# Kernel optimization log

Measured on AMD Instinct MI355X. Metric: run time of the kernel, lower is better.

## Reference

```python
import jax, jax.numpy as jnp
import numpy as np
from jax.scipy.special import logsumexp

NEG = -1.0e7  # -QUASI_INF
B, T = 8, 16
QALL, QRES, QARG = 256, 128, 192
STATE, VOCAB = 256, 10000


def setup_inputs() -> dict:
    key = jax.random.key(0)
    ks = jax.random.split(key, 24)
    def rn(k, shape, s=0.1):
        return jax.random.normal(k, shape, dtype=jnp.float32) * s
    z = lambda *s: jnp.zeros(s, jnp.float32)
    return {
        "words": jax.random.randint(ks[0], (B, T), 0, VOCAB),
        "nt_emb": rn(ks[1], (QALL, STATE), 1.0),
        "W_emit": rn(ks[2], (STATE, VOCAB)),
        "b_emit": z(VOCAB),
        "rule_W": rn(ks[3], (QRES, 2 * QARG)),
        "rule_b": z(2 * QARG),
        "assoc": rn(ks[4], (QRES, QARG)),
        "root_w": rn(ks[5], (QALL,)),
        "root_b": z(QALL),
        "sw1": rn(ks[6], (STATE, STATE)), "sb1": z(STATE),
        "r1w1": rn(ks[7], (STATE, STATE)), "r1b1": z(STATE),
        "r1w2": rn(ks[8], (STATE, STATE)), "r1b2": z(STATE),
        "r2w1": rn(ks[9], (STATE, STATE)), "r2b1": z(STATE),
        "r2w2": rn(ks[10], (STATE, STATE)), "r2b2": z(STATE),
        "sw2": rn(ks[11], (STATE, 2)), "sb2": z(2),
        "lfunc_ixs": jax.random.randint(ks[12], (QRES, QARG), 0, QALL),
        "rfunc_ixs": jax.random.randint(ks[13], (QRES, QARG), 0, QALL),
        "argpc_2_pc": jax.random.randint(ks[14], (QARG,), 0, QALL),
        "res_2_all": jnp.arange(QRES, dtype=jnp.int32),
        "larg_mask": z(QRES, QARG),
        "rarg_mask": z(QRES, QARG),
    }


def _residual(x, w1, b1, w2, b2):
    return x + jax.nn.relu(jax.nn.relu(x @ w1 + b1) @ w2 + b2)


def _forward(words, nt_emb, W_emit, b_emit, rule_W, rule_b, assoc, root_w, root_b,
             sw1, sb1, r1w1, r1b1, r1w2, r1b2, r2w1, r2b1, r2w2, r2b2, sw2, sb2,
             lfunc_ixs, rfunc_ixs, argpc_2_pc, res_2_all, larg_mask, rarg_mask):
    Bb, Tt = words.shape
    qall = nt_emb.shape[0]
    qres, qarg = assoc.shape
    # rule_mlp applied to fake_emb = eye(qres): logits are just W + b, then log-softmax
    G = jax.nn.log_softmax(rule_W + rule_b, axis=-1) + jnp.concatenate([assoc, assoc], axis=1)
    G_larg = G[:, :qarg] + larg_mask   # argument child on the left
    G_rarg = G[:, qarg:] + rarg_mask   # argument child on the right
    # split/emit binary decision per category (split_mlp over nt_emb)
    h = nt_emb @ sw1 + sb1
    h = _residual(h, r1w1, r1b1, r1w2, r1b2)
    h = _residual(h, r2w1, r2b1, r2w2, r2b2)
    split_scores = jax.nn.log_softmax(h @ sw2 + sb2, axis=-1)  # [qall, 2]
    # emission log-probs (word model: dense projection + log-softmax over vocab)
    emit_lp = jax.nn.log_softmax(nt_emb @ W_emit + b_emit, axis=-1)  # [qall, V]
    term = jnp.moveaxis(emit_lp[:, words], 0, -1) + split_scores[:, 1]  # [B, T, qall]
    # inside chart: chart[len-1, start] -> [B, qall] log inside scores
    chart = jnp.full((Tt, Tt, Bb, qall), NEG, dtype=jnp.float32)
    chart = chart.at[0].set(jnp.swapaxes(term, 0, 1))
    split0 = split_scores[res_2_all, 0]  # split prob of result predcats
    for ell in range(2, Tt + 1):  # DP recurrence over span length (structural)
        n = Tt - ell + 1
        kk = np.arange(1, ell)
        st = np.arange(n)
        lefts = chart[kk - 1, :n]  # [S, n, B, qall]
        rights = chart[(ell - kk - 1)[:, None], st[None, :] + kk[:, None]]  # [S, n, B, qall]
        # functor on left, argument on right: lfunc_ixs[res,arg] -> functor predcat
        sc1 = lefts[..., lfunc_ixs] + rights[..., argpc_2_pc][..., None, :] + G_rarg
        # argument on left, functor on right
        sc2 = lefts[..., argpc_2_pc][..., None, :] + rights[..., rfunc_ixs] + G_larg
        parent = jnp.logaddexp(logsumexp(sc1, axis=(0, 4)), logsumexp(sc2, axis=(0, 4)))  # [n, B, qres]
        parent = parent + split0
        full = jnp.full((n, Bb, qall), NEG, dtype=jnp.float32).at[:, :, res_2_all].set(parent)
        chart = chart.at[ell - 1, :n].set(full)
    root_lp = jax.nn.log_softmax(root_w + root_b)  # root_mlp over eye(1)
    return logsumexp(chart[Tt - 1, 0] + root_lp, axis=-1)  # [B] sentence log-likelihoods


def reference(words, nt_emb, W_emit, b_emit, rule_W, rule_b, assoc, root_w, root_b,
              sw1, sb1, r1w1, r1b1, r1w2, r1b2, r2w1, r2b1, r2w2, r2b2, sw2, sb2,
              lfunc_ixs, rfunc_ixs, argpc_2_pc, res_2_all, larg_mask, rarg_mask):
    return _forward(words, nt_emb, W_emit, b_emit, rule_W, rule_b, assoc, root_w, root_b,
                    sw1, sb1, r1w1, r1b1, r1w2, r1b2, r2w1, r2b1, r2w2, r2b2, sw2, sb2,
                    lfunc_ixs, rfunc_ixs, argpc_2_pc, res_2_all, larg_mask, rarg_mask)
```

## Files before the change

kernel.cpp:

```cpp
#include <hip/hip_runtime.h>
#include <math.h>

#define NEGV -10000000.0f

constexpr int B_ = 8, T_ = 16;
constexpr int QALL = 256, QRES = 128, QARG = 192;
constexpr int STATE = 256, VOCAB = 10000;
constexpr int WT = 64;
constexpr int NWT = (VOCAB + WT - 1) / WT;
constexpr int JS = 4;

constexpr size_t OFF_CHART = 0;
constexpr size_t CHART_SZ  = (size_t)T_ * T_ * B_ * QALL;
constexpr size_t OFF_EGR   = OFF_CHART + CHART_SZ;
constexpr size_t OFF_EGL   = OFF_EGR + (size_t)QARG * QRES;
constexpr size_t OFF_LF    = OFF_EGL + (size_t)QARG * QRES;
constexpr size_t OFF_RF    = OFF_LF + (size_t)QARG * QRES;
constexpr size_t OFF_S0    = OFF_RF + (size_t)QARG * QRES;
constexpr size_t OFF_S1    = OFF_S0 + QALL;
constexpr size_t OFF_LSE   = OFF_S1 + QALL;
constexpr size_t OFF_PMIT  = OFF_LSE + QALL;
constexpr size_t OFF_PSEM  = OFF_PMIT + (size_t)NWT * QALL;
constexpr int    PMAXP     = 704;
constexpr size_t OFF_P0S   = OFF_PMIT;
constexpr size_t OFF_P0M   = OFF_P0S + (size_t)PMAXP * QRES;
constexpr size_t OFF_P1S   = OFF_P0M + PMAXP;
constexpr size_t OFF_P1M   = OFF_P1S + (size_t)PMAXP * QRES;
constexpr size_t OFF_RAW   = OFF_P1S;

__device__ __forceinline__ size_t chIdx(int ell, int s, int b) {
    return OFF_CHART + ((size_t)((ell * 16 + s) * 8 + b)) * 256;
}

__device__ __forceinline__ float waveMax(float v) {
    #pragma unroll
    for (int m = 32; m >= 1; m >>= 1) v = fmaxf(v, __shfl_xor(v, m, 64));
    return v;
}
__device__ __forceinline__ float waveSum(float v) {
    #pragma unroll
    for (int m = 32; m >= 1; m >>= 1) v += __shfl_xor(v, m, 64);
    return v;
}
__device__ __forceinline__ float blockMax(float v, float* scr, int nw) {
    int lane = threadIdx.x & 63, w = threadIdx.x >> 6;
    v = waveMax(v);
    if (lane == 0) scr[w] = v;
    __syncthreads();
    float r = scr[0];
    for (int i = 1; i < nw; i++) r = fmaxf(r, scr[i]);
    __syncthreads();
    return r;
}
__device__ __forceinline__ float blockSum(float v, float* scr, int nw) {
    int lane = threadIdx.x & 63, w = threadIdx.x >> 6;
    v = waveSum(v);
    if (lane == 0) scr[w] = v;
    __syncthreads();
    float r = 0.f;
    for (int i = 0; i < nw; i++) r += scr[i];
    __syncthreads();
    return r;
}

__global__ __launch_bounds__(192) void prep_g_kernel(
        const float* __restrict__ rule_W, const float* __restrict__ rule_b,
        const float* __restrict__ assoc,
        const float* __restrict__ larg_mask, const float* __restrict__ rarg_mask,
        const int* __restrict__ lfunc, const int* __restrict__ rfunc,
        float* __restrict__ ws) {
    __shared__ float scr[4];
    int r = blockIdx.x;
    int j = threadIdx.x;
    float v0 = rule_W[r * 2 * QARG + j] + rule_b[j];
    float v1 = rule_W[r * 2 * QARG + QARG + j] + rule_b[QARG + j];
    float m = blockMax(fmaxf(v0, v1), scr, 3);
    float s = blockSum(expf(v0 - m) + expf(v1 - m), scr, 3);
    float l = m + logf(s);
    float av = assoc[r * QARG + j];
    float gl = v0 - l + av + larg_mask[r * QARG + j];
    float gr = v1 - l + av + rarg_mask[r * QARG + j];
    ws[OFF_EGL + (size_t)j * QRES + r] = expf(gl);
    ws[OFF_EGR + (size_t)j * QRES + r] = expf(gr);
    ((int*)ws)[OFF_LF + (size_t)j * QRES + r] = lfunc[r * QARG + j];
    ((int*)ws)[OFF_RF + (size_t)j * QRES + r] = rfunc[r * QARG + j];
}

#define MLP_MATVEC(INBUF, W, RES) do {                                          \
    float acc_ = 0.f;                                                           \
    _Pragma("unroll 16")                                                        \
    for (int s_ = 0; s_ < 64; s_++)                                             \
        acc_ += INBUF[s0 + s_] * W[(s0 + s_) * STATE + col];                    \
    part[t] = acc_;                                                             \
    __syncthreads();                                                            \
    RES = part[col] + part[STATE + col] + part[2 * STATE + col]                 \
        + part[3 * STATE + col];                                                \
} while (0)

__global__ __launch_bounds__(1024) void mlp_kernel(
        const float* __restrict__ nt_emb,
        const float* __restrict__ sw1, const float* __restrict__ sb1,
        const float* __restrict__ r1w1, const float* __restrict__ r1b1,
        const float* __restrict__ r1w2, const float* __restrict__ r1b2,
        const float* __restrict__ r2w1, const float* __restrict__ r2b1,
        const float* __restrict__ r2w2, const float* __restrict__ r2b2,
        const float* __restrict__ sw2, const float* __restrict__ sb2,
        float* __restrict__ ws) {
    __shared__ float xin[STATE], hbuf[STATE], tbuf[STATE];
    __shared__ float part[4 * STATE];
    __shared__ float scr[16];
    int a = blockIdx.x, t = threadIdx.x;
    int col = t & 255;
    int grp = t >> 8;
    int s0 = grp * 64;
    if (t < STATE) xin[t] = nt_emb[a * STATE + t];
    __syncthreads();
    float r;
    MLP_MATVEC(xin, sw1, r);
    if (grp == 0) hbuf[col] = r + sb1[col];
    __syncthreads();
    MLP_MATVEC(hbuf, r1w1, r);
    if (grp == 0) tbuf[col] = fmaxf(r + r1b1[col], 0.f);
    __syncthreads();
    MLP_MATVEC(tbuf, r1w2, r);
    if (grp == 0) hbuf[col] += fmaxf(r + r1b2[col], 0.f);
    __syncthreads();
    MLP_MATVEC(hbuf, r2w1, r);
    if (grp == 0) tbuf[col] = fmaxf(r + r2b1[col], 0.f);
    __syncthreads();
    MLP_MATVEC(tbuf, r2w2, r);
    if (grp == 0) hbuf[col] += fmaxf(r + r2b2[col], 0.f);
    __syncthreads();
    float hv = (t < STATE) ? hbuf[t] : 0.f;
    float v0 = (t < STATE) ? hv * sw2[t * 2 + 0] : 0.f;
    float v1 = (t < STATE) ? hv * sw2[t * 2 + 1] : 0.f;
    float u0 = blockSum(v0, scr, 16) + sb2[0];
    float u1 = blockSum(v1, scr, 16) + sb2[1];
    if (t == 0) {
        float mm = fmaxf(u0, u1);
        float l = mm + logf(expf(u0 - mm) + expf(u1 - mm));
        ws[OFF_S0 + a] = u0 - l;
        ws[OFF_S1 + a] = u1 - l;
    }
}

__global__ __launch_bounds__(256) void emit_kernel(
        const int* __restrict__ words,
        const float* __restrict__ nt_emb, const float* __restrict__ W_emit,
        const float* __restrict__ b_emit, float* __restrict__ ws) {
    __shared__ float As[2][16][64];
    __shared__ float Bs[2][16][64];
    __shared__ float redM[64][16], redS[64][16];
    __shared__ int sw[128];
    int wt = blockIdx.x, at = blockIdx.y;
    int t = threadIdx.x;
    int tx = t & 15, ty = t >> 4;
    if (t < 128) sw[t] = words[t];
    int wbase = wt * WT, abase = at * 64;
    int idx = t * 4;
    int akk = idx & 15, aaa = idx >> 4;
    int bkk = idx >> 6, bww = idx & 63;
    const float* Aptr = &nt_emb[(size_t)(abase + aaa) * STATE + akk];
    int bw = wbase + bww;
    bool bfull = (bw + 3 < VOCAB);

    {
        float4 av = *(const float4*)(Aptr + 0);
        float4 bv;
        const float* src = &W_emit[(size_t)bkk * VOCAB + bw];
        if (bfull) bv = *(const float4*)src;
        else {
            float tv[4];
            #pragma unroll
            for (int q = 0; q < 4; q++) tv[q] = (bw + q < VOCAB) ? src[q] : 0.f;
            bv = make_float4(tv[0], tv[1], tv[2], tv[3]);
        }
        As[0][akk + 0][aaa] = av.x; As[0][akk + 1][aaa] = av.y;
        As[0][akk + 2][aaa] = av.z; As[0][akk + 3][aaa] = av.w;
        *(float4*)&Bs[0][bkk][bww] = bv;
    }
    __syncthreads();

    float acc[4][4];
    #pragma unroll
    for (int i = 0; i < 4; i++)
        #pragma unroll
        for (int j = 0; j < 4; j++) acc[i][j] = 0.f;

    for (int step = 0; step < 16; step++) {
        int cur = step & 1;
        float4 nav, nbv;
        bool more = (step + 1 < 16);
        if (more) {
            nav = *(const float4*)(Aptr + (step + 1) * 16);
            const float* src = &W_emit[(size_t)((step + 1) * 16 + bkk) * VOCAB + bw];
            if (bfull) nbv = *(const float4*)src;
            else {
                float tv[4];
                #pragma unroll
                for (int q = 0; q < 4; q++) tv[q] = (bw + q < VOCAB) ? src[q] : 0.f;
                nbv = make_float4(tv[0], tv[1], tv[2], tv[3]);
            }
        }
        #pragma unroll
        for (int kk = 0; kk < 16; kk++) {
            float a4[4], b4[4];
            #pragma unroll
            for (int i = 0; i < 4; i++) a4[i] = As[cur][kk][ty * 4 + i];
            #pragma unroll
            for (int j = 0; j < 4; j++) b4[j] = Bs[cur][kk][tx * 4 + j];
            #pragma unroll
            for (int i = 0; i < 4; i++)
                #pragma unroll
                for (int j = 0; j < 4; j++) acc[i][j] += a4[i] * b4[j];
        }
        if (more) {
            int nb = cur ^ 1;
            As[nb][akk + 0][aaa] = nav.x; As[nb][akk + 1][aaa] = nav.y;
            As[nb][akk + 2][aaa] = nav.z; As[nb][akk + 3][aaa] = nav.w;
            *(float4*)&Bs[nb][bkk][bww] = nbv;
        }
        __syncthreads();
    }

    float be[4];
    #pragma unroll
    for (int j = 0; j < 4; j++) {
        int w = wbase + tx * 4 + j;
        be[j] = (w < VOCAB) ? b_emit[w] : 0.f;
    }
    #pragma unroll
    for (int i = 0; i < 4; i++)
        #pragma unroll
        for (int j = 0; j < 4; j++) {
            int w = wbase + tx * 4 + j;
            if (w < VOCAB) acc[i][j] += be[j];
        }
    for (int i2 = 0; i2 < 128; i2++) {
        int loc = sw[i2] - wbase;
        if (loc >= 0 && loc < WT && (loc >> 2) == tx) {
            int j = loc & 3;
            #pragma unroll
            for (int i = 0; i < 4; i++)
                ws[OFF_RAW + (size_t)i2 * QALL + abase + ty * 4 + i] = acc[i][j];
        }
    }
    #pragma unroll
    for (int i = 0; i < 4; i++) {
        float mloc = -3.0e38f;
        #pragma unroll
        for (int j = 0; j < 4; j++) {
            int w = wbase + tx * 4 + j;
            if (w < VOCAB) mloc = fmaxf(mloc, acc[i][j]);
        }
        float sloc = 0.f;
        #pragma unroll
        for (int j = 0; j < 4; j++) {
            int w = wbase + tx * 4 + j;
            if (w < VOCAB) sloc += expf(acc[i][j] - mloc);
        }
        redM[ty * 4 + i][tx] = mloc;
        redS[ty * 4 + i][tx] = sloc;
    }
    __syncthreads();
    if (t < 64) {
        float M = -3.0e38f;
        #pragma unroll
        for (int i = 0; i < 16; i++) M = fmaxf(M, redM[t][i]);
        float S = 0.f;
        #pragma unroll
        for (int i = 0; i < 16; i++) S += redS[t][i] * expf(redM[t][i] - M);
        ws[OFF_PMIT + (size_t)wt * QALL + abase + t] = M;
        ws[OFF_PSEM + (size_t)wt * QALL + abase + t] = S;
    }
}

__global__ __launch_bounds__(256) void lse_kernel(float* __restrict__ ws) {
    int a = threadIdx.x;
    float M = -3.0e38f;
    for (int wt = 0; wt < NWT; wt++) M = fmaxf(M, ws[OFF_PMIT + (size_t)wt * QALL + a]);
    float S = 0.f;
    for (int wt = 0; wt < NWT; wt++)
        S += ws[OFF_PSEM + (size_t)wt * QALL + a] * expf(ws[OFF_PMIT + (size_t)wt * QALL + a] - M);
    ws[OFF_LSE + a] = M + logf(S);
}

__global__ __launch_bounds__(256) void chart0_kernel(float* __restrict__ ws) {
    int blk = blockIdx.x;
    int b = blk >> 4, tp = blk & 15;
    int a = threadIdx.x;
    float val = ws[OFF_RAW + (size_t)blk * QALL + a] - ws[OFF_LSE + a] + ws[OFF_S1 + a];
    ws[chIdx(0, tp, b) + a] = val;
}

__device__ __forceinline__ void reconRow(float* row, const float* __restrict__ ws,
                                         size_t prevS, size_t prevM, int cellp, int KCp,
                                         const int* __restrict__ res2all) {
    int t = threadIdx.x;
    int np = JS * KCp;
    size_t base = (size_t)cellp * np;
    if (t < 256) row[t] = NEGV;
    float M = -3.0e38f;
    for (int p = 0; p < np; p++) M = fmaxf(M, ws[prevM + base + p]);
    __syncthreads();
    if (t < QRES) {
        float S = 0.f;
        for (int p = 0; p < np; p++)
            S += expf(ws[prevM + base + p] - M) * ws[prevS + (base + p) * QRES + t];
        row[res2all[t]] = logf(S) + M + ws[OFF_S0 + res2all[t]];
    }
    __syncthreads();
}

template<int ELL>
__global__ __launch_bounds__(512) void level_k(float* __restrict__ ws,
                                               const int* __restrict__ argpc,
                                               const int* __restrict__ res2all) {
    __shared__ __align__(16) float rowL[4][256], rowR[4][256];
    __shared__ __align__(16) float eB0[4][48], eB1[4][48];
    __shared__ float mLs[4], mRs[4];
    __shared__ float Sred[512];
    __shared__ float outrow[256];

    constexpr int K = ELL - 1;
    constexpr int KC = (K + 3) >> 2;
    constexpr int matCount = (ELL >= 3) ? (T_ - ELL + 2) * 8 : 0;
    constexpr int ellp = ELL - 1;
    constexpr int KCp = (ellp - 1 + 3) >> 2;
    constexpr size_t prevS = (ellp & 1) ? OFF_P1S : OFF_P0S;
    constexpr size_t prevM = (ellp & 1) ? OFF_P1M : OFF_P0M;
    constexpr size_t curS  = (ELL & 1) ? OFF_P1S : OFF_P0S;
    constexpr size_t curM  = (ELL & 1) ? OFF_P1M : OFF_P0M;

    int t = threadIdx.x;
    int bid = blockIdx.x;

    if (bid < matCount) {
        int cellp = bid;
        int sp = cellp >> 3, bp = cellp & 7;
        reconRow(outrow, ws, prevS, prevM, cellp, KCp, res2all);
        if (t < 256) ws[chIdx(ellp - 1, sp, bp) + t] = outrow[t];
        return;
    }

    int aid = bid - matCount;
    int kc = aid % KC;
    int rem = aid / KC;
    int jq = rem & (JS - 1);
    int cell = rem >> 2;
    int s = cell >> 3, b = cell & 7;
    int k0 = kc * 4 + 1;
    int kn = min(4, K - kc * 4);
    int j0 = jq * 48;
    int side = t >> 8, u = t & 255;

    for (int kp = 0; kp < kn; kp++) {
        int k = k0 + kp;
        bool Lprev = (ELL >= 3) && (k == K);
        bool Rprev = (ELL >= 3) && (k == 1);
        if (!Lprev && side == 0) rowL[kp][u] = ws[chIdx(k - 1, s, b) + u];
        if (!Rprev && side == 1) rowR[kp][u] = ws[chIdx(ELL - k - 1, s + k, b) + u];
    }
    for (int kp = 0; kp < kn; kp++) {
        int k = k0 + kp;
        if ((ELL >= 3) && (k == K)) reconRow(&rowL[kp][0], ws, prevS, prevM, s * 8 + b, KCp, res2all);
        if ((ELL >= 3) && (k == 1)) reconRow(&rowR[kp][0], ws, prevS, prevM, (s + 1) * 8 + b, KCp, res2all);
    }
    __syncthreads();

    int w = t >> 6, lane = t & 63;
    if (w < 2 * kn) {
        int kp = w >> 1;
        const float* pr = (w & 1) ? &rowR[kp][0] : &rowL[kp][0];
        float v = fmaxf(fmaxf(pr[lane], pr[lane + 64]), fmaxf(pr[lane + 128], pr[lane + 192]));
        v = waveMax(v);
        if (lane == 0) { if (w & 1) mRs[kp] = v; else mLs[kp] = v; }
    }
    __syncthreads();
    float mc = -3.0e38f;
    for (int kp = 0; kp < kn; kp++) mc = fmaxf(mc, mLs[kp] + mRs[kp]);

    {
        int kp = t >> 7;
        int jj = t & 127;
        if (kp < kn) {
            if (jj < 48) {
                int ap = argpc[j0 + jj];
                eB0[kp][jj] = expf(rowR[kp][ap] - (mc - mLs[kp]));
            } else if (jj >= 64 && jj < 112) {
                int j2 = jj - 64;
                int ap = argpc[j0 + j2];
                eB1[kp][j2] = expf(rowL[kp][ap] - (mc - mRs[kp]));
            }
        }
    }
    __syncthreads();

    for (int kp = 0; kp < kn; kp++) {
        if (side == 0) rowL[kp][u] = expf(rowL[kp][u] - mLs[kp]);
        else           rowR[kp][u] = expf(rowR[kp][u] - mRs[kp]);
    }
    __syncthreads();

    int r = t & 127, sub = t >> 7;
    int which = sub >> 1;
    int jbase = (sub & 1) * 24;
    const float* eGT = ws + (which == 0 ? OFF_EGR : OFF_EGL);
    const int* idxT = ((const int*)ws) + (which == 0 ? OFF_LF : OFF_RF);
    const float (*gA)[256] = which ? rowR : rowL;
    const float (*gB)[48]  = which ? eB1 : eB0;
    float acc = 0.f;
    for (int jc = 0; jc < 24; jc += 4) {
        int jj = jbase + jc;
        int j = j0 + jj;
        float g0 = eGT[(size_t)(j + 0) * QRES + r];
        float g1 = eGT[(size_t)(j + 1) * QRES + r];
        float g2 = eGT[(size_t)(j + 2) * QRES + r];
        float g3 = eGT[(size_t)(j + 3) * QRES + r];
        int i0 = idxT[(size_t)(j + 0) * QRES + r];
        int i1 = idxT[(size_t)(j + 1) * QRES + r];
        int i2 = idxT[(size_t)(j + 2) * QRES + r];
        int i3 = idxT[(size_t)(j + 3) * QRES + r];
        float t0 = 0.f, t1 = 0.f, t2 = 0.f, t3 = 0.f;
        for (int kp = 0; kp < kn; kp++) {
            const float* gs = gA[kp];
            float4 e4 = *(const float4*)&gB[kp][jj];
            t0 += gs[i0] * e4.x;
            t1 += gs[i1] * e4.y;
            t2 += gs[i2] * e4.z;
            t3 += gs[i3] * e4.w;
        }
        acc += g0 * t0 + g1 * t1 + g2 * t2 + g3 * t3;
    }
    Sred[t] = acc;
    __syncthreads();
    if (t < QRES) {
        float S = Sred[t] + Sred[128 + t] + Sred[256 + t] + Sred[384 + t];
        ws[curS + (size_t)aid * QRES + t] = S;
    }
    if (t == 0) ws[curM + aid] = mc;
}

__global__ __launch_bounds__(256) void root_kernel(const float* __restrict__ root_w,
                                                   const float* __restrict__ root_b,
                                                   const float* __restrict__ ws,
                                                   const int* __restrict__ res2all,
                                                   float* __restrict__ out) {
    int b = blockIdx.x, t = threadIdx.x;
    __shared__ float scr[4];
    __shared__ float outrow[256];
    {
        int np = JS * 4;
        size_t base = (size_t)b * np;
        outrow[t] = NEGV;
        float M = -3.0e38f;
        for (int p = 0; p < np; p++) M = fmaxf(M, ws[OFF_P0M + base + p]);
        __syncthreads();
        if (t < QRES) {
            float S = 0.f;
            for (int p = 0; p < np; p++)
                S += expf(ws[OFF_P0M + base + p] - M) * ws[OFF_P0S + (base + p) * QRES + t];
            outrow[res2all[t]] = logf(S) + M + ws[OFF_S0 + res2all[t]];
        }
        __syncthreads();
    }
    float rv = root_w[t] + root_b[t];
    float mroot = blockMax(rv, scr, 4);
    float sroot = blockSum(expf(rv - mroot), scr, 4);
    float lroot = mroot + logf(sroot);
    float v = outrow[t] + rv - lroot;
    float m2 = blockMax(v, scr, 4);
    float s2 = blockSum(expf(v - m2), scr, 4);
    if (t == 0) out[b] = m2 + logf(s2);
}

template<int ELL>
static inline void launch_level(float* ws, const int* argpc, const int* res2all,
                                hipStream_t stream) {
    constexpr int n = T_ - ELL + 1;
    constexpr int K = ELL - 1, KC = (K + 3) / 4;
    constexpr int matCount = (ELL >= 3) ? (n + 1) * 8 : 0;
    constexpr int accCount = n * 8 * JS * KC;
    level_k<ELL><<<dim3(matCount + accCount), dim3(512), 0, stream>>>(ws, argpc, res2all);
}

extern "C" void kernel_launch(void* const* d_in, const int* in_sizes, int n_in,
                              void* d_out, int out_size, void* d_ws, size_t ws_size,
                              hipStream_t stream) {
    const int*   words   = (const int*)  d_in[0];
    const float* nt_emb  = (const float*)d_in[1];
    const float* W_emit  = (const float*)d_in[2];
    const float* b_emit  = (const float*)d_in[3];
    const float* rule_W  = (const float*)d_in[4];
    const float* rule_b  = (const float*)d_in[5];
    const float* assoc   = (const float*)d_in[6];
    const float* root_w  = (const float*)d_in[7];
    const float* root_b  = (const float*)d_in[8];
    const float* sw1     = (const float*)d_in[9];
    const float* sb1     = (const float*)d_in[10];
    const float* r1w1    = (const float*)d_in[11];
    const float* r1b1    = (const float*)d_in[12];
    const float* r1w2    = (const float*)d_in[13];
    const float* r1b2    = (const float*)d_in[14];
    const float* r2w1    = (const float*)d_in[15];
    const float* r2b1    = (const float*)d_in[16];
    const float* r2w2    = (const float*)d_in[17];
    const float* r2b2    = (const float*)d_in[18];
    const float* sw2     = (const float*)d_in[19];
    const float* sb2     = (const float*)d_in[20];
    const int*   lfunc   = (const int*)  d_in[21];
    const int*   rfunc   = (const int*)  d_in[22];
    const int*   argpc   = (const int*)  d_in[23];
    const int*   res2all = (const int*)  d_in[24];
    const float* larg_m  = (const float*)d_in[25];
    const float* rarg_m  = (const float*)d_in[26];
    float* ws  = (float*)d_ws;
    float* out = (float*)d_out;

    prep_g_kernel<<<dim3(QRES), dim3(QARG), 0, stream>>>(rule_W, rule_b, assoc, larg_m, rarg_m,
                                                         lfunc, rfunc, ws);
    mlp_kernel<<<dim3(QALL), dim3(1024), 0, stream>>>(nt_emb, sw1, sb1, r1w1, r1b1, r1w2, r1b2,
                                                      r2w1, r2b1, r2w2, r2b2, sw2, sb2, ws);
    emit_kernel<<<dim3(NWT, QALL / 64), dim3(256), 0, stream>>>(words, nt_emb, W_emit, b_emit, ws);
    lse_kernel<<<dim3(1), dim3(256), 0, stream>>>(ws);
    chart0_kernel<<<dim3(B_ * T_), dim3(256), 0, stream>>>(ws);

    launch_level<2>(ws, argpc, res2all, stream);
    launch_level<3>(ws, argpc, res2all, stream);
    launch_level<4>(ws, argpc, res2all, stream);
    launch_level<5>(ws, argpc, res2all, stream);
    launch_level<6>(ws, argpc, res2all, stream);
    launch_level<7>(ws, argpc, res2all, stream);
    launch_level<8>(ws, argpc, res2all, stream);
    launch_level<9>(ws, argpc, res2all, stream);
    launch_level<10>(ws, argpc, res2all, stream);
    launch_level<11>(ws, argpc, res2all, stream);
    launch_level<12>(ws, argpc, res2all, stream);
    launch_level<13>(ws, argpc, res2all, stream);
    launch_level<14>(ws, argpc, res2all, stream);
    launch_level<15>(ws, argpc, res2all, stream);
    launch_level<16>(ws, argpc, res2all, stream);

    root_kernel<<<dim3(B_), dim3(256), 0, stream>>>(root_w, root_b, ws, res2all, out);
}
```

Before: 367.5 us.

## Fuse prep/MLP and lse/chart0 kernels, hoist G loads into registers

Merges the rule-prep kernel into the MLP kernel as extra blocks and folds the single-block LSE reduction into chart0, so two kernel launches and their serialization points disappear. Each chart0 block now recomputes the LSE over all vocab tiles, which duplicates that reduction 128 times. In the level kernel, the G/index gathers and argpc loads are hoisted into registers before the row loads, overlapping global latency with earlier work. reconRow is also templated on the partial count so its loops can be unrolled. The register arrays raise register pressure.

```diff
diff --git a/kernel.cpp b/kernel.cpp
--- a/kernel.cpp
+++ b/kernel.cpp
@@ -63,29 +63,6 @@
     return r;
 }
 
-__global__ __launch_bounds__(192) void prep_g_kernel(
-        const float* __restrict__ rule_W, const float* __restrict__ rule_b,
-        const float* __restrict__ assoc,
-        const float* __restrict__ larg_mask, const float* __restrict__ rarg_mask,
-        const int* __restrict__ lfunc, const int* __restrict__ rfunc,
-        float* __restrict__ ws) {
-    __shared__ float scr[4];
-    int r = blockIdx.x;
-    int j = threadIdx.x;
-    float v0 = rule_W[r * 2 * QARG + j] + rule_b[j];
-    float v1 = rule_W[r * 2 * QARG + QARG + j] + rule_b[QARG + j];
-    float m = blockMax(fmaxf(v0, v1), scr, 3);
-    float s = blockSum(expf(v0 - m) + expf(v1 - m), scr, 3);
-    float l = m + logf(s);
-    float av = assoc[r * QARG + j];
-    float gl = v0 - l + av + larg_mask[r * QARG + j];
-    float gr = v1 - l + av + rarg_mask[r * QARG + j];
-    ws[OFF_EGL + (size_t)j * QRES + r] = expf(gl);
-    ws[OFF_EGR + (size_t)j * QRES + r] = expf(gr);
-    ((int*)ws)[OFF_LF + (size_t)j * QRES + r] = lfunc[r * QARG + j];
-    ((int*)ws)[OFF_RF + (size_t)j * QRES + r] = rfunc[r * QARG + j];
-}
-
 #define MLP_MATVEC(INBUF, W, RES) do {                                          \
     float acc_ = 0.f;                                                           \
     _Pragma("unroll 16")                                                        \
@@ -97,7 +74,7 @@
         + part[3 * STATE + col];                                                \
 } while (0)
 
-__global__ __launch_bounds__(1024) void mlp_kernel(
+__global__ __launch_bounds__(1024) void pre_kernel(
         const float* __restrict__ nt_emb,
         const float* __restrict__ sw1, const float* __restrict__ sb1,
         const float* __restrict__ r1w1, const float* __restrict__ r1b1,
@@ -105,42 +82,69 @@
         const float* __restrict__ r2w1, const float* __restrict__ r2b1,
         const float* __restrict__ r2w2, const float* __restrict__ r2b2,
         const float* __restrict__ sw2, const float* __restrict__ sb2,
+        const float* __restrict__ rule_W, const float* __restrict__ rule_b,
+        const float* __restrict__ assoc,
+        const float* __restrict__ larg_mask, const float* __restrict__ rarg_mask,
+        const int* __restrict__ lfunc, const int* __restrict__ rfunc,
         float* __restrict__ ws) {
     __shared__ float xin[STATE], hbuf[STATE], tbuf[STATE];
     __shared__ float part[4 * STATE];
     __shared__ float scr[16];
-    int a = blockIdx.x, t = threadIdx.x;
-    int col = t & 255;
-    int grp = t >> 8;
-    int s0 = grp * 64;
-    if (t < STATE) xin[t] = nt_emb[a * STATE + t];
-    __syncthreads();
-    float r;
-    MLP_MATVEC(xin, sw1, r);
-    if (grp == 0) hbuf[col] = r + sb1[col];
-    __syncthreads();
-    MLP_MATVEC(hbuf, r1w1, r);
-    if (grp == 0) tbuf[col] = fmaxf(r + r1b1[col], 0.f);
-    __syncthreads();
-    MLP_MATVEC(tbuf, r1w2, r);
-    if (grp == 0) hbuf[col] += fmaxf(r + r1b2[col], 0.f);
-    __syncthreads();
-    MLP_MATVEC(hbuf, r2w1, r);
-    if (grp == 0) tbuf[col] = fmaxf(r + r2b1[col], 0.f);
-    __syncthreads();
-    MLP_MATVEC(tbuf, r2w2, r);
-    if (grp == 0) hbuf[col] += fmaxf(r + r2b2[col], 0.f);
-    __syncthreads();
-    float hv = (t < STATE) ? hbuf[t] : 0.f;
-    float v0 = (t < STATE) ? hv * sw2[t * 2 + 0] : 0.f;
-    float v1 = (t < STATE) ? hv * sw2[t * 2 + 1] : 0.f;
-    float u0 = blockSum(v0, scr, 16) + sb2[0];
-    float u1 = blockSum(v1, scr, 16) + sb2[1];
-    if (t == 0) {
-        float mm = fmaxf(u0, u1);
-        float l = mm + logf(expf(u0 - mm) + expf(u1 - mm));
-        ws[OFF_S0 + a] = u0 - l;
-        ws[OFF_S1 + a] = u1 - l;
+    int t = threadIdx.x;
+    if (blockIdx.x < QALL) {
+        int a = blockIdx.x;
+        int col = t & 255;
+        int grp = t >> 8;
+        int s0 = grp * 64;
+        if (t < STATE) xin[t] = nt_emb[a * STATE + t];
+        __syncthreads();
+        float r;
+        MLP_MATVEC(xin, sw1, r);
+        if (grp == 0) hbuf[col] = r + sb1[col];
+        __syncthreads();
+        MLP_MATVEC(hbuf, r1w1, r);
+        if (grp == 0) tbuf[col] = fmaxf(r + r1b1[col], 0.f);
+        __syncthreads();
+        MLP_MATVEC(tbuf, r1w2, r);
+        if (grp == 0) hbuf[col] += fmaxf(r + r1b2[col], 0.f);
+        __syncthreads();
+        MLP_MATVEC(hbuf, r2w1, r);
+        if (grp == 0) tbuf[col] = fmaxf(r + r2b1[col], 0.f);
+        __syncthreads();
+        MLP_MATVEC(tbuf, r2w2, r);
+        if (grp == 0) hbuf[col] += fmaxf(r + r2b2[col], 0.f);
+        __syncthreads();
+        float hv = (t < STATE) ? hbuf[t] : 0.f;
+        float v0 = (t < STATE) ? hv * sw2[t * 2 + 0] : 0.f;
+        float v1 = (t < STATE) ? hv * sw2[t * 2 + 1] : 0.f;
+        float u0 = blockSum(v0, scr, 16) + sb2[0];
+        float u1 = blockSum(v1, scr, 16) + sb2[1];
+        if (t == 0) {
+            float mm = fmaxf(u0, u1);
+            float l = mm + logf(expf(u0 - mm) + expf(u1 - mm));
+            ws[OFF_S0 + a] = u0 - l;
+            ws[OFF_S1 + a] = u1 - l;
+        }
+    } else {
+        int r = blockIdx.x - QALL;
+        int j = t;
+        float v0 = -3.0e38f, v1 = -3.0e38f;
+        if (t < QARG) {
+            v0 = rule_W[r * 2 * QARG + j] + rule_b[j];
+            v1 = rule_W[r * 2 * QARG + QARG + j] + rule_b[QARG + j];
+        }
+        float m = blockMax(fmaxf(v0, v1), scr, 16);
+        float s = blockSum((t < QARG) ? (expf(v0 - m) + expf(v1 - m)) : 0.f, scr, 16);
+        if (t < QARG) {
+            float l = m + logf(s);
+            float av = assoc[r * QARG + j];
+            float gl = v0 - l + av + larg_mask[r * QARG + j];
+            float gr = v1 - l + av + rarg_mask[r * QARG + j];
+            ws[OFF_EGL + (size_t)j * QRES + r] = expf(gl);
+            ws[OFF_EGR + (size_t)j * QRES + r] = expf(gr);
+            ((int*)ws)[OFF_LF + (size_t)j * QRES + r] = lfunc[r * QARG + j];
+            ((int*)ws)[OFF_RF + (size_t)j * QRES + r] = rfunc[r * QARG + j];
+        }
     }
 }
 
@@ -275,38 +279,39 @@
     }
 }
 
-__global__ __launch_bounds__(256) void lse_kernel(float* __restrict__ ws) {
+__global__ __launch_bounds__(256) void chart0_kernel(float* __restrict__ ws) {
+    int blk = blockIdx.x;
+    int b = blk >> 4, tp = blk & 15;
     int a = threadIdx.x;
     float M = -3.0e38f;
     for (int wt = 0; wt < NWT; wt++) M = fmaxf(M, ws[OFF_PMIT + (size_t)wt * QALL + a]);
     float S = 0.f;
     for (int wt = 0; wt < NWT; wt++)
         S += ws[OFF_PSEM + (size_t)wt * QALL + a] * expf(ws[OFF_PMIT + (size_t)wt * QALL + a] - M);
-    ws[OFF_LSE + a] = M + logf(S);
-}
-
-__global__ __launch_bounds__(256) void chart0_kernel(float* __restrict__ ws) {
-    int blk = blockIdx.x;
-    int b = blk >> 4, tp = blk & 15;
-    int a = threadIdx.x;
-    float val = ws[OFF_RAW + (size_t)blk * QALL + a] - ws[OFF_LSE + a] + ws[OFF_S1 + a];
+    float lse = M + logf(S);
+    float val = ws[OFF_RAW + (size_t)blk * QALL + a] - lse + ws[OFF_S1 + a];
     ws[chIdx(0, tp, b) + a] = val;
 }
 
+template<int NP>
 __device__ __forceinline__ void reconRow(float* row, const float* __restrict__ ws,
-                                         size_t prevS, size_t prevM, int cellp, int KCp,
+                                         size_t prevS, size_t prevM, int cellp,
                                          const int* __restrict__ res2all) {
     int t = threadIdx.x;
-    int np = JS * KCp;
-    size_t base = (size_t)cellp * np;
+    size_t base = (size_t)cellp * NP;
+    float Mp[NP];
+    #pragma unroll
+    for (int p = 0; p < NP; p++) Mp[p] = ws[prevM + base + p];
+    float M = -3.0e38f;
+    #pragma unroll
+    for (int p = 0; p < NP; p++) M = fmaxf(M, Mp[p]);
     if (t < 256) row[t] = NEGV;
-    float M = -3.0e38f;
-    for (int p = 0; p < np; p++) M = fmaxf(M, ws[prevM + base + p]);
     __syncthreads();
     if (t < QRES) {
         float S = 0.f;
-        for (int p = 0; p < np; p++)
-            S += expf(ws[prevM + base + p] - M) * ws[prevS + (base + p) * QRES + t];
+        #pragma unroll
+        for (int p = 0; p < NP; p++)
+            S += expf(Mp[p] - M) * ws[prevS + (base + p) * QRES + t];
         row[res2all[t]] = logf(S) + M + ws[OFF_S0 + res2all[t]];
     }
     __syncthreads();
@@ -325,8 +330,9 @@
     constexpr int K = ELL - 1;
     constexpr int KC = (K + 3) >> 2;
     constexpr int matCount = (ELL >= 3) ? (T_ - ELL + 2) * 8 : 0;
+    constexpr int KCp = (ELL >= 3) ? ((ELL - 2 + 3) >> 2) : 1;
+    constexpr int NPp = JS * KCp;
     constexpr int ellp = ELL - 1;
-    constexpr int KCp = (ellp - 1 + 3) >> 2;
     constexpr size_t prevS = (ellp & 1) ? OFF_P1S : OFF_P0S;
     constexpr size_t prevM = (ellp & 1) ? OFF_P1M : OFF_P0M;
     constexpr size_t curS  = (ELL & 1) ? OFF_P1S : OFF_P0S;
@@ -335,12 +341,14 @@
     int t = threadIdx.x;
     int bid = blockIdx.x;
 
-    if (bid < matCount) {
-        int cellp = bid;
-        int sp = cellp >> 3, bp = cellp & 7;
-        reconRow(outrow, ws, prevS, prevM, cellp, KCp, res2all);
-        if (t < 256) ws[chIdx(ellp - 1, sp, bp) + t] = outrow[t];
-        return;
+    if constexpr (ELL >= 3) {
+        if (bid < matCount) {
+            int cellp = bid;
+            int sp = cellp >> 3, bp = cellp & 7;
+            reconRow<NPp>(outrow, ws, prevS, prevM, cellp, res2all);
+            if (t < 256) ws[chIdx(ellp - 1, sp, bp) + t] = outrow[t];
+            return;
+        }
     }
 
     int aid = bid - matCount;
@@ -354,6 +362,23 @@
     int j0 = jq * 48;
     int side = t >> 8, u = t & 255;
 
+    int r = t & 127, sub = t >> 7;
+    int which = sub >> 1;
+    int jbase = (sub & 1) * 24;
+    const float* eGT = ws + (which == 0 ? OFF_EGR : OFF_EGL);
+    const int* idxT = ((const int*)ws) + (which == 0 ? OFF_LF : OFF_RF);
+    float gReg[24]; int iReg[24];
+    #pragma unroll
+    for (int jc = 0; jc < 24; jc++) {
+        int j = j0 + jbase + jc;
+        gReg[jc] = eGT[(size_t)j * QRES + r];
+        iReg[jc] = idxT[(size_t)j * QRES + r];
+    }
+    int kp3 = t >> 7, jj3 = t & 127;
+    int ap3 = 0; bool g3a = (jj3 < 48), g3b = (jj3 >= 64 && jj3 < 112);
+    if (g3a) ap3 = argpc[j0 + jj3];
+    else if (g3b) ap3 = argpc[j0 + jj3 - 64];
+
     for (int kp = 0; kp < kn; kp++) {
         int k = k0 + kp;
         bool Lprev = (ELL >= 3) && (k == K);
@@ -361,10 +386,12 @@
         if (!Lprev && side == 0) rowL[kp][u] = ws[chIdx(k - 1, s, b) + u];
         if (!Rprev && side == 1) rowR[kp][u] = ws[chIdx(ELL - k - 1, s + k, b) + u];
     }
-    for (int kp = 0; kp < kn; kp++) {
-        int k = k0 + kp;
-        if ((ELL >= 3) && (k == K)) reconRow(&rowL[kp][0], ws, prevS, prevM, s * 8 + b, KCp, res2all);
-        if ((ELL >= 3) && (k == 1)) reconRow(&rowR[kp][0], ws, prevS, prevM, (s + 1) * 8 + b, KCp, res2all);
+    if constexpr (ELL >= 3) {
+        for (int kp = 0; kp < kn; kp++) {
+            int k = k0 + kp;
+            if (k == K) reconRow<NPp>(&rowL[kp][0], ws, prevS, prevM, s * 8 + b, res2all);
+            if (k == 1) reconRow<NPp>(&rowR[kp][0], ws, prevS, prevM, (s + 1) * 8 + b, res2all);
+        }
     }
     __syncthreads();
 
@@ -380,19 +407,9 @@
     float mc = -3.0e38f;
     for (int kp = 0; kp < kn; kp++) mc = fmaxf(mc, mLs[kp] + mRs[kp]);
 
-    {
-        int kp = t >> 7;
-        int jj = t & 127;
-        if (kp < kn) {
-            if (jj < 48) {
-                int ap = argpc[j0 + jj];
-                eB0[kp][jj] = expf(rowR[kp][ap] - (mc - mLs[kp]));
-            } else if (jj >= 64 && jj < 112) {
-                int j2 = jj - 64;
-                int ap = argpc[j0 + j2];
-                eB1[kp][j2] = expf(rowL[kp][ap] - (mc - mRs[kp]));
-            }
-        }
+    if (kp3 < kn) {
+        if (g3a)      eB0[kp3][jj3]      = expf(rowR[kp3][ap3] - (mc - mLs[kp3]));
+        else if (g3b) eB1[kp3][jj3 - 64] = expf(rowL[kp3][ap3] - (mc - mRs[kp3]));
     }
     __syncthreads();
 
@@ -402,35 +419,22 @@
     }
     __syncthreads();
 
-    int r = t & 127, sub = t >> 7;
-    int which = sub >> 1;
-    int jbase = (sub & 1) * 24;
-    const float* eGT = ws + (which == 0 ? OFF_EGR : OFF_EGL);
-    const int* idxT = ((const int*)ws) + (which == 0 ? OFF_LF : OFF_RF);
     const float (*gA)[256] = which ? rowR : rowL;
     const float (*gB)[48]  = which ? eB1 : eB0;
     float acc = 0.f;
+    #pragma unroll
     for (int jc = 0; jc < 24; jc += 4) {
         int jj = jbase + jc;
-        int j = j0 + jj;
-        float g0 = eGT[(size_t)(j + 0) * QRES + r];
-        float g1 = eGT[(size_t)(j + 1) * QRES + r];
-        float g2 = eGT[(size_t)(j + 2) * QRES + r];
-        float g3 = eGT[(size_t)(j + 3) * QRES + r];
-        int i0 = idxT[(size_t)(j + 0) * QRES + r];
-        int i1 = idxT[(size_t)(j + 1) * QRES + r];
-        int i2 = idxT[(size_t)(j + 2) * QRES + r];
-        int i3 = idxT[(size_t)(j + 3) * QRES + r];
         float t0 = 0.f, t1 = 0.f, t2 = 0.f, t3 = 0.f;
         for (int kp = 0; kp < kn; kp++) {
             const float* gs = gA[kp];
             float4 e4 = *(const float4*)&gB[kp][jj];
-            t0 += gs[i0] * e4.x;
-            t1 += gs[i1] * e4.y;
-            t2 += gs[i2] * e4.z;
-            t3 += gs[i3] * e4.w;
-        }
-        acc += g0 * t0 + g1 * t1 + g2 * t2 + g3 * t3;
+            t0 += gs[iReg[jc + 0]] * e4.x;
+            t1 += gs[iReg[jc + 1]] * e4.y;
+            t2 += gs[iReg[jc + 2]] * e4.z;
+            t3 += gs[iReg[jc + 3]] * e4.w;
+        }
+        acc += gReg[jc + 0] * t0 + gReg[jc + 1] * t1 + gReg[jc + 2] * t2 + gReg[jc + 3] * t3;
     }
     Sred[t] = acc;
     __syncthreads();
@@ -517,12 +521,10 @@
     float* ws  = (float*)d_ws;
     float* out = (float*)d_out;
 
-    prep_g_kernel<<<dim3(QRES), dim3(QARG), 0, stream>>>(rule_W, rule_b, assoc, larg_m, rarg_m,
-                                                         lfunc, rfunc, ws);
-    mlp_kernel<<<dim3(QALL), dim3(1024), 0, stream>>>(nt_emb, sw1, sb1, r1w1, r1b1, r1w2, r1b2,
-                                                      r2w1, r2b1, r2w2, r2b2, sw2, sb2, ws);
+    pre_kernel<<<dim3(QALL + QRES), dim3(1024), 0, stream>>>(
+        nt_emb, sw1, sb1, r1w1, r1b1, r1w2, r1b2, r2w1, r2b1, r2w2, r2b2, sw2, sb2,
+        rule_W, rule_b, assoc, larg_m, rarg_m, lfunc, rfunc, ws);
     emit_kernel<<<dim3(NWT, QALL / 64), dim3(256), 0, stream>>>(words, nt_emb, W_emit, b_emit, ws);
-    lse_kernel<<<dim3(1), dim3(256), 0, stream>>>(ws);
     chart0_kernel<<<dim3(B_ * T_), dim3(256), 0, stream>>>(ws);
 
     launch_level<2>(ws, argpc, res2all, stream);
```

After: 459.8 us. +25.1%, slower.
